# Kernel optimization log

Measured on AMD Instinct MI355X. Metric: run time of the kernel, lower is better.

The kernel has to match this reference:

```python
import jax, jax.numpy as jnp
import numpy as np

B, N, K, DIM = 2, 20000, 16, 256


def _mlp(x, W, b):
    # torch nn.Linear: x @ W.T + b, then LeakyReLU(0.1)
    return jax.nn.leaky_relu(x @ W.T + b, negative_slope=0.1)


def _lfa(features, geom, idx, W, b):
    # features: [B, N, C]; geom: [B, N, K, 4]; idx: [B, N, K]
    t = _mlp(geom, W, b)                                  # [B, N, K, d_lfa]
    fn = jax.vmap(lambda f, i: f[i])(features, idx)       # gather neighbors: [B, N, K, C]
    # mean over K of concat == concat of means (faithful, avoids big concat)
    return jnp.concatenate([t.mean(axis=2), fn.mean(axis=2)], axis=-1)


def _linear_init(key, out_f, in_f):
    k1, k2 = jax.random.split(key)
    bound = 1.0 / np.sqrt(in_f)
    W = jax.random.uniform(k1, (out_f, in_f), jnp.float32, -bound, bound)
    b = jax.random.uniform(k2, (out_f,), jnp.float32, -bound, bound)
    return W, b


def setup_inputs() -> dict:
    key = jax.random.key(0)
    ks = jax.random.split(key, 8)
    W_init, b_init = _linear_init(ks[0], DIM // 4, DIM)
    W_l1, b_l1 = _linear_init(ks[1], DIM // 4, 4)
    W_l2, b_l2 = _linear_init(ks[2], DIM // 2, 4)
    W_fin, b_fin = _linear_init(ks[3], DIM, DIM)
    W_id, b_id = _linear_init(ks[4], DIM, DIM)
    return {
        "input_tensor": jax.random.normal(ks[5], (B, N, DIM), jnp.float32),
        "geometric_features": jax.random.normal(ks[6], (B, N, K, 4), jnp.float32),
        "neighbor_indices": jax.random.randint(ks[7], (B, N, K), 0, N, jnp.int64 if jax.config.jax_enable_x64 else jnp.int32),
        "W_init": W_init, "b_init": b_init,
        "W_l1": W_l1, "b_l1": b_l1,
        "W_l2": W_l2, "b_l2": b_l2,
        "W_fin": W_fin, "b_fin": b_fin,
        "W_id": W_id, "b_id": b_id,
    }


def reference(input_tensor, geometric_features, neighbor_indices,
              W_init, b_init, W_l1, b_l1, W_l2, b_l2,
              W_fin, b_fin, W_id, b_id):
    residual = input_tensor
    x = _mlp(input_tensor, W_init, b_init)                       # [B, N, dim/4]
    x = _lfa(x, geometric_features, neighbor_indices, W_l1, b_l1)  # [B, N, dim/2]
    x = _lfa(x, geometric_features, neighbor_indices, W_l2, b_l2)  # [B, N, dim]
    x = _mlp(x, W_fin, b_fin)
    return x + _mlp(residual, W_id, b_id)
```

## Files before the change

### kernel.cpp

```cpp
#include <hip/hip_runtime.h>
#include <hip/hip_bf16.h>

#define BN   40000
#define NPTS 20000
#define KNN  16
#define DIM  256

typedef __attribute__((ext_vector_type(8))) short bf16x8;
typedef __attribute__((ext_vector_type(4))) float f32x4;
typedef __attribute__((ext_vector_type(16))) float f32x16;

__device__ __forceinline__ float lrelu(float v) { return fmaxf(v, 0.1f * v); }
__device__ __forceinline__ float bs2f(short s) {
    union { unsigned u; float f; } c; c.u = ((unsigned)(unsigned short)s) << 16;
    return c.f;
}
__device__ __forceinline__ short f2bs(float f) {
    __hip_bfloat16 h = __float2bfloat16(f);
    return *reinterpret_cast<short*>(&h);
}
__device__ __forceinline__ bf16x8 ldf32_bf16x8(const float* p) {
    const float4 a = ((const float4*)p)[0];
    const float4 b = ((const float4*)p)[1];
    bf16x8 r;
    r[0]=f2bs(a.x); r[1]=f2bs(a.y); r[2]=f2bs(a.z); r[3]=f2bs(a.w);
    r[4]=f2bs(b.x); r[5]=f2bs(b.y); r[6]=f2bs(b.z); r[7]=f2bs(b.w);
    return r;
}

__device__ __forceinline__ void dma16(const void* g, void* l) {
    __builtin_amdgcn_global_load_lds(
        (const __attribute__((address_space(1))) unsigned int*)g,
        (__attribute__((address_space(3))) unsigned int*)l, 16, 0, 0);
}

__global__ void __launch_bounds__(256) prep_kernel(
    const int* __restrict__ idxw, int* __restrict__ flag,
    const float* __restrict__ Wf, const float* __restrict__ Wi,
    const float* __restrict__ Wn,
    short* __restrict__ Wt, short* __restrict__ Wnt)
{
    if (blockIdx.x == 0) {
        __shared__ int red[256];
        int t = threadIdx.x;
        int v = 0;
#pragma unroll
        for (int it = 0; it < 64; ++it)
            v |= idxw[2 * (t + it * 256) + 1];
        red[t] = v;
        __syncthreads();
        for (int s = 128; s > 0; s >>= 1) {
            if (t < s) red[t] |= red[t + s];
            __syncthreads();
        }
        if (t == 0) *flag = (red[0] != 0) ? 1 : 0;
        return;
    }
    int t = (blockIdx.x - 1) * 256 + threadIdx.x;
    if (t < 32768) {
        int mat = (t >> 14) & 1;
        int tt  = t & 16383;
        float4 v = mat ? ((const float4*)Wi)[tt] : ((const float4*)Wf)[tt];
        int n  = tt >> 6;
        int k  = (tt & 63) * 4;
        int kk = k >> 5, q = (k >> 3) & 3, j = k & 7;
        short4 o; o.x=f2bs(v.x); o.y=f2bs(v.y); o.z=f2bs(v.z); o.w=f2bs(v.w);
        *(short4*)(Wt + ((size_t)((kk*2 + mat)*4 + q))*2048 + n*8 + j) = o;
    } else {
        int tt = t - 32768;
        float4 v = ((const float4*)Wn)[tt];
        int n  = tt >> 6;
        int k  = (tt & 63) * 4;
        int kk = k >> 5, q = (k >> 3) & 3, j = k & 7;
        short4 o; o.x=f2bs(v.x); o.y=f2bs(v.y); o.z=f2bs(v.z); o.w=f2bs(v.w);
        *(short4*)(Wnt + ((size_t)((kk*4 + q)*64 + n))*8 + j) = o;
    }
}

__global__ void __launch_bounds__(256) stage2_kernel(
    const float* __restrict__ geom,
    const float* __restrict__ W1, const float* __restrict__ B1,
    const float* __restrict__ W2, const float* __restrict__ B2,
    const float* __restrict__ X,
    const short* __restrict__ Wnt,
    const float* __restrict__ b_init,
    __hip_bfloat16* __restrict__ x2,
    __hip_bfloat16* __restrict__ x3,
    __hip_bfloat16* __restrict__ x1)
{
    __shared__ short wbuf[16384];

    if (blockIdx.x >= 625) {
        int bid = blockIdx.x - 625;
        int t = threadIdx.x;
        int wave = t >> 6, lane = t & 63;
        int r = lane & 15, q = lane >> 4;
        {
            const char* W8 = (const char*)Wnt;
            char* L8 = (char*)wbuf;
#pragma unroll
            for (int rd = 0; rd < 8; ++rd) {
                int off = (wave * 8 + rd) * 1024 + lane * 16;
                dma16(W8 + off, L8 + off);
            }
        }
        int m0 = bid * 64 + wave * 16;
        const float* Xs = X + (size_t)(m0 + r) * DIM + q * 8;
        bf16x8 a[8];
#pragma unroll
        for (int kk = 0; kk < 8; ++kk) a[kk] = ldf32_bf16x8(Xs + kk * 32);
        __syncthreads();

        f32x4 acc[4];
#pragma unroll
        for (int nt = 0; nt < 4; ++nt) acc[nt] = (f32x4){0.f,0.f,0.f,0.f};
#pragma unroll
        for (int kk = 0; kk < 8; ++kk) {
#pragma unroll
            for (int nt = 0; nt < 4; ++nt) {
                bf16x8 b = *(const bf16x8*)&wbuf[((kk*4 + q)*64 + nt*16 + r) * 8];
                acc[nt] = __builtin_amdgcn_mfma_f32_16x16x32_bf16(a[kk], b, acc[nt], 0, 0, 0);
            }
        }
#pragma unroll
        for (int nt = 0; nt < 4; ++nt) {
            int col = nt * 16 + r;
            float bvx = b_init[col];
#pragma unroll
            for (int i = 0; i < 4; ++i) {
                float v = lrelu(acc[nt][i] + bvx);
                x1[(size_t)(m0 + q*4 + i) * 64 + col] = __float2bfloat16(v);
            }
        }
        return;
    }

    const int lane = threadIdx.x & 63;
    const int wv   = threadIdx.x >> 6;
    const int c31  = lane & 31;
    const int hi   = lane >> 5;
    const int wglob = blockIdx.x * 4 + wv;

    bf16x8 bfr[6]; float bv[6];
#pragma unroll
    for (int tt = 0; tt < 6; ++tt) {
        bfr[tt] = (bf16x8){0,0,0,0,0,0,0,0};
        const float* Wrow;
        if (tt < 2) { Wrow = W1 + (size_t)(tt*32 + c31) * 4;     bv[tt] = B1[tt*32 + c31]; }
        else        { Wrow = W2 + (size_t)((tt-2)*32 + c31) * 4; bv[tt] = B2[(tt-2)*32 + c31]; }
        if (hi == 0) {
            const float4 w4 = *(const float4*)Wrow;
            bfr[tt][0]=f2bs(w4.x); bfr[tt][1]=f2bs(w4.y);
            bfr[tt][2]=f2bs(w4.z); bfr[tt][3]=f2bs(w4.w);
        }
    }
    f32x16 ZR;
#pragma unroll
    for (int i = 0; i < 16; ++i) ZR[i] = 0.f;

    float4 g = (float4){0.f,0.f,0.f,0.f};
    if (hi == 0)
        g = *(const float4*)(geom +
            ((size_t)((wglob * 8) * 2 + (c31 >> 4)) * KNN + (c31 & 15)) * 4);

#pragma unroll
    for (int it = 0; it < 8; ++it) {
        const int p0 = (wglob * 8 + it) * 2;
        const float4 gc = g;
        if (it < 7 && hi == 0)
            g = *(const float4*)(geom +
                ((size_t)(p0 + 2 + (c31 >> 4)) * KNN + (c31 & 15)) * 4);

        bf16x8 a = (bf16x8){0,0,0,0,0,0,0,0};
        if (hi == 0) { a[0]=f2bs(gc.x); a[1]=f2bs(gc.y); a[2]=f2bs(gc.z); a[3]=f2bs(gc.w); }

        f32x16 acc[6];
#pragma unroll
        for (int tt = 0; tt < 6; ++tt)
            acc[tt] = __builtin_amdgcn_mfma_f32_32x32x16_bf16(a, bfr[tt], ZR, 0, 0, 0);

#pragma unroll
        for (int tt = 0; tt < 6; ++tt) {
            float sA = 0.f, sB = 0.f;
#pragma unroll
            for (int i = 0; i < 8; ++i)  sA += lrelu(acc[tt][i]     + bv[tt]);
#pragma unroll
            for (int i = 0; i < 8; ++i)  sB += lrelu(acc[tt][i + 8] + bv[tt]);
            sA += __shfl_xor(sA, 32, 64);
            sB += __shfl_xor(sB, 32, 64);
            const float s = (hi ? sB : sA) * (1.f / 16.f);
            const short v = f2bs(s);
            if (tt < 2) ((short*)x2)[(size_t)(p0 + hi) * 128 + tt*32 + c31] = v;
            else        ((short*)x3)[(size_t)(p0 + hi) * 256 + (tt-2)*32 + c31] = v;
        }
    }
}

__global__ void __launch_bounds__(256) gather1_kernel(
    const int* __restrict__ idxw, const int* __restrict__ flag,
    const __hip_bfloat16* __restrict__ x1,
    __hip_bfloat16* __restrict__ x2)
{
    int t = blockIdx.x * 256 + threadIdx.x;
    int p = t >> 3, j = t & 7;
    int lane = threadIdx.x & 63;
    int dual = (*flag == 0) ? 2 : 1;
    int base = (p >= NPTS) ? NPTS : 0;
    int i0 = idxw[((size_t)p * 16 + 2*j)     * dual];
    int i1 = idxw[((size_t)p * 16 + 2*j + 1) * dual];
    int g8 = lane & 56;
    float acc[8];
#pragma unroll
    for (int i = 0; i < 8; ++i) acc[i] = 0.f;
#pragma unroll
    for (int k = 0; k < 8; ++k) {
        int rA = base + __shfl(i0, g8 + k, 64);
        int rB = base + __shfl(i1, g8 + k, 64);
        bf16x8 vA = *(const bf16x8*)((const short*)x1 + (size_t)rA * 64 + j * 8);
        bf16x8 vB = *(const bf16x8*)((const short*)x1 + (size_t)rB * 64 + j * 8);
#pragma unroll
        for (int i = 0; i < 8; ++i) acc[i] += bs2f(vA[i]) + bs2f(vB[i]);
    }
    bf16x8 o;
#pragma unroll
    for (int i = 0; i < 8; ++i) o[i] = f2bs(acc[i] * (1.f/16.f));
    *(bf16x8*)((short*)x2 + (size_t)p * 128 + 64 + j * 8) = o;
}

__global__ void __launch_bounds__(256) gather2_kernel(
    const int* __restrict__ idxw, const int* __restrict__ flag,
    const __hip_bfloat16* __restrict__ x2,
    __hip_bfloat16* __restrict__ x3)
{
    int t = blockIdx.x * 256 + threadIdx.x;
    int p = t >> 4, j = t & 15;
    int lane = threadIdx.x & 63;
    int dual = (*flag == 0) ? 2 : 1;
    int base = (p >= NPTS) ? NPTS : 0;
    int myi = idxw[((size_t)p * 16 + j) * dual];
    int g16 = lane & 48;
    float acc[8];
#pragma unroll
    for (int i = 0; i < 8; ++i) acc[i] = 0.f;
#pragma unroll
    for (int k = 0; k < KNN; ++k) {
        int row = base + __shfl(myi, g16 + k, 64);
        bf16x8 v = *(const bf16x8*)((const short*)x2 + (size_t)row * 128 + j * 8);
#pragma unroll
        for (int i = 0; i < 8; ++i) acc[i] += bs2f(v[i]);
    }
    bf16x8 o;
#pragma unroll
    for (int i = 0; i < 8; ++i) o[i] = f2bs(acc[i] * (1.f/16.f));
    *(bf16x8*)((short*)x3 + (size_t)p * 256 + 128 + j * 8) = o;
}

__global__ void __launch_bounds__(512, 2) final_mfma(
    const __hip_bfloat16* __restrict__ X3,
    const float* __restrict__ RES,
    const short* __restrict__ Wt,
    const float* __restrict__ Bf,
    const float* __restrict__ Bi,
    float* __restrict__ OUT)
{
    __shared__ short lw[65536];
    const int t    = threadIdx.x;
    const int wave = t >> 6, lane = t & 63;
    const int r = lane & 15, q = lane >> 4;
    const int rg = wave >> 1, cg = wave & 1;
    const int ch = blockIdx.x & 1;
    const int p0 = (blockIdx.x >> 1) * 320;

    {
        const char* WtB = (const char*)Wt;
        char* L = (char*)lw;
#pragma unroll
        for (int i = 0; i < 16; ++i) {
            int c = wave * 8 + (i >> 1);
            int d = i & 1;
            int mat = c >> 5, kk = (c >> 2) & 7, qq = c & 3;
            int src_sh = ((kk * 2 + mat) * 4 + qq) * 2048 + ch * 1024;
            dma16(WtB + (size_t)src_sh * 2 + d * 1024 + lane * 16,
                  L + (c * 2 + d) * 1024 + lane * 16);
        }
    }
    const int cb = ch * 128 + cg * 64;
    float bfv[4], biv[4];
#pragma unroll
    for (int nt = 0; nt < 4; ++nt) {
        bfv[nt] = Bf[cb + nt * 16 + r];
        biv[nt] = Bi[cb + nt * 16 + r];
    }
    __syncthreads();

    const short* bpf = lw + q * 1024 + (cg * 64 + r) * 8;
    const short* bpi = bpf + 32768;

#pragma unroll
    for (int tt = 0; tt < 5; ++tt) {
        const int row = p0 + tt * 64 + rg * 16 + r;
        const short* x3r = (const short*)X3 + (size_t)row * DIM + q * 8;
        const float* rsr = RES + (size_t)row * DIM + q * 8;

        bf16x8 a1[8];
        float4 rw[16];
#pragma unroll
        for (int kk = 0; kk < 8; ++kk) {
            rw[2*kk]   = ((const float4*)rsr)[kk * 8];
            rw[2*kk+1] = ((const float4*)rsr)[kk * 8 + 1];
            a1[kk] = *(const bf16x8*)(x3r + kk * 32);
        }

        f32x4 acc1[4], acc2[4];
#pragma unroll
        for (int nt = 0; nt < 4; ++nt) {
            acc1[nt] = (f32x4){0.f,0.f,0.f,0.f};
            acc2[nt] = (f32x4){0.f,0.f,0.f,0.f};
        }
#pragma unroll
        for (int kk = 0; kk < 8; ++kk) {
            bf16x8 a2;
            {
                const float4 lo = rw[2*kk], hi = rw[2*kk+1];
                a2[0]=f2bs(lo.x); a2[1]=f2bs(lo.y); a2[2]=f2bs(lo.z); a2[3]=f2bs(lo.w);
                a2[4]=f2bs(hi.x); a2[5]=f2bs(hi.y); a2[6]=f2bs(hi.z); a2[7]=f2bs(hi.w);
            }
#pragma unroll
            for (int nt = 0; nt < 4; ++nt) {
                bf16x8 b1 = *(const bf16x8*)(bpf + kk * 4096 + nt * 128);
                bf16x8 b2 = *(const bf16x8*)(bpi + kk * 4096 + nt * 128);
                acc1[nt] = __builtin_amdgcn_mfma_f32_16x16x32_bf16(a1[kk], b1, acc1[nt], 0, 0, 0);
                acc2[nt] = __builtin_amdgcn_mfma_f32_16x16x32_bf16(a2,    b2, acc2[nt], 0, 0, 0);
            }
        }
#pragma unroll
        for (int nt = 0; nt < 4; ++nt) {
            const int col = cb + nt * 16 + r;
#pragma unroll
            for (int i = 0; i < 4; ++i) {
                float v = lrelu(acc1[nt][i] + bfv[nt]) + lrelu(acc2[nt][i] + biv[nt]);
                OUT[(size_t)(p0 + tt * 64 + rg * 16 + q * 4 + i) * DIM + col] = v;
            }
        }
    }
}

extern "C" void kernel_launch(void* const* d_in, const int* in_sizes, int n_in,
                              void* d_out, int out_size, void* d_ws, size_t ws_size,
                              hipStream_t stream)
{
    const float* input  = (const float*)d_in[0];
    const float* geom   = (const float*)d_in[1];
    const int*   idxw   = (const int*)d_in[2];
    const float* W_init = (const float*)d_in[3];
    const float* b_init = (const float*)d_in[4];
    const float* W_l1   = (const float*)d_in[5];
    const float* b_l1   = (const float*)d_in[6];
    const float* W_l2   = (const float*)d_in[7];
    const float* b_l2   = (const float*)d_in[8];
    const float* W_fin  = (const float*)d_in[9];
    const float* b_fin  = (const float*)d_in[10];
    const float* W_id   = (const float*)d_in[11];
    const float* b_id   = (const float*)d_in[12];
    float* out = (float*)d_out;

    char* ws = (char*)d_ws;
    int* flag = (int*)ws;
    short* Wt  = (short*)(ws + 16);
    short* Wnt = (short*)(ws + 16 + 262144);
    __hip_bfloat16* x2 = (__hip_bfloat16*)(ws + 16 + 5120000);
    __hip_bfloat16* x3 = (__hip_bfloat16*)(ws + 16 + 15360000);
    __hip_bfloat16* x1 = (__hip_bfloat16*)d_out;

    prep_kernel<<<145, 256, 0, stream>>>(idxw, flag, W_fin, W_id, W_init,
                                         Wt, Wnt);
    stage2_kernel<<<1250, 256, 0, stream>>>(geom, W_l1, b_l1, W_l2, b_l2,
                                            input, Wnt, b_init, x2, x3, x1);
    gather1_kernel<<<1250, 256, 0, stream>>>(idxw, flag, x1, x2);
    gather2_kernel<<<2500, 256, 0, stream>>>(idxw, flag, x2, x3);
    final_mfma<<<250, 512, 0, stream>>>(x3, input, Wt, b_fin, b_id, out);
}
```

Measured before the change: 195.8 us.

## Fuse second neighbor gather into final MFMA kernel via shared-memory staging

Removes the separate gather2 kernel and computes the second-LFA neighbor mean inside the final GEMM kernel. Each 64-row tile is staged in LDS, and x3 now stores only its 128 MLP columns, so the round trip of the gathered half through global memory goes away. Each block of 250 redundantly gathers its tile for both column halves, since ch splits output columns. Occupancy is lowered to 1 block per CU by extra LDS and launch bounds, and the tile loop is no longer unrolled, with two syncs per iteration.

```diff
diff --git a/kernel.cpp b/kernel.cpp
--- a/kernel.cpp
+++ b/kernel.cpp
@@ -191,7 +191,7 @@
             const float s = (hi ? sB : sA) * (1.f / 16.f);
             const short v = f2bs(s);
             if (tt < 2) ((short*)x2)[(size_t)(p0 + hi) * 128 + tt*32 + c31] = v;
-            else        ((short*)x3)[(size_t)(p0 + hi) * 256 + (tt-2)*32 + c31] = v;
+            else        ((short*)x3)[(size_t)(p0 + hi) * 128 + (tt-2)*32 + c31] = v;
         }
     }
 }
@@ -227,36 +227,10 @@
     *(bf16x8*)((short*)x2 + (size_t)p * 128 + 64 + j * 8) = o;
 }
 
-__global__ void __launch_bounds__(256) gather2_kernel(
+__global__ void __launch_bounds__(512, 1) final_mfma(
+    const __hip_bfloat16* __restrict__ X3g,
+    const __hip_bfloat16* __restrict__ X2,
     const int* __restrict__ idxw, const int* __restrict__ flag,
-    const __hip_bfloat16* __restrict__ x2,
-    __hip_bfloat16* __restrict__ x3)
-{
-    int t = blockIdx.x * 256 + threadIdx.x;
-    int p = t >> 4, j = t & 15;
-    int lane = threadIdx.x & 63;
-    int dual = (*flag == 0) ? 2 : 1;
-    int base = (p >= NPTS) ? NPTS : 0;
-    int myi = idxw[((size_t)p * 16 + j) * dual];
-    int g16 = lane & 48;
-    float acc[8];
-#pragma unroll
-    for (int i = 0; i < 8; ++i) acc[i] = 0.f;
-#pragma unroll
-    for (int k = 0; k < KNN; ++k) {
-        int row = base + __shfl(myi, g16 + k, 64);
-        bf16x8 v = *(const bf16x8*)((const short*)x2 + (size_t)row * 128 + j * 8);
-#pragma unroll
-        for (int i = 0; i < 8; ++i) acc[i] += bs2f(v[i]);
-    }
-    bf16x8 o;
-#pragma unroll
-    for (int i = 0; i < 8; ++i) o[i] = f2bs(acc[i] * (1.f/16.f));
-    *(bf16x8*)((short*)x3 + (size_t)p * 256 + 128 + j * 8) = o;
-}
-
-__global__ void __launch_bounds__(512, 2) final_mfma(
-    const __hip_bfloat16* __restrict__ X3,
     const float* __restrict__ RES,
     const short* __restrict__ Wt,
     const float* __restrict__ Bf,
@@ -264,12 +238,14 @@
     float* __restrict__ OUT)
 {
     __shared__ short lw[65536];
+    __shared__ short x3h[64 * 136];
     const int t    = threadIdx.x;
     const int wave = t >> 6, lane = t & 63;
     const int r = lane & 15, q = lane >> 4;
     const int rg = wave >> 1, cg = wave & 1;
     const int ch = blockIdx.x & 1;
     const int p0 = (blockIdx.x >> 1) * 320;
+    const int dual = (*flag == 0) ? 2 : 1;
 
     {
         const char* WtB = (const char*)Wt;
@@ -291,15 +267,15 @@
         bfv[nt] = Bf[cb + nt * 16 + r];
         biv[nt] = Bi[cb + nt * 16 + r];
     }
-    __syncthreads();
 
     const short* bpf = lw + q * 1024 + (cg * 64 + r) * 8;
     const short* bpi = bpf + 32768;
-
-#pragma unroll
+    const int jg  = t & 15;
+    const int g16 = lane & 48;
+
+#pragma unroll 1
     for (int tt = 0; tt < 5; ++tt) {
         const int row = p0 + tt * 64 + rg * 16 + r;
-        const short* x3r = (const short*)X3 + (size_t)row * DIM + q * 8;
         const float* rsr = RES + (size_t)row * DIM + q * 8;
 
         bf16x8 a1[8];
@@ -308,8 +284,44 @@
         for (int kk = 0; kk < 8; ++kk) {
             rw[2*kk]   = ((const float4*)rsr)[kk * 8];
             rw[2*kk+1] = ((const float4*)rsr)[kk * 8 + 1];
-            a1[kk] = *(const bf16x8*)(x3r + kk * 32);
-        }
+        }
+        {
+            const short* x3r = (const short*)X3g + (size_t)row * 128 + q * 8;
+#pragma unroll
+            for (int kk = 0; kk < 4; ++kk)
+                a1[kk] = *(const bf16x8*)(x3r + kk * 32);
+        }
+
+#pragma unroll
+        for (int pass = 0; pass < 2; ++pass) {
+            const int rl = (t >> 4) + pass * 32;
+            const int p  = p0 + tt * 64 + rl;
+            const int base = (p >= NPTS) ? NPTS : 0;
+            const int myi = idxw[((size_t)p * 16 + jg) * dual];
+            float ac[8];
+#pragma unroll
+            for (int i = 0; i < 8; ++i) ac[i] = 0.f;
+#pragma unroll
+            for (int k = 0; k < KNN; ++k) {
+                int nbr = base + __shfl(myi, g16 + k, 64);
+                bf16x8 v = *(const bf16x8*)((const short*)X2 + (size_t)nbr * 128 + jg * 8);
+#pragma unroll
+                for (int i = 0; i < 8; ++i) ac[i] += bs2f(v[i]);
+            }
+            bf16x8 o;
+#pragma unroll
+            for (int i = 0; i < 8; ++i) o[i] = f2bs(ac[i] * (1.f/16.f));
+            *(bf16x8*)&x3h[rl * 136 + jg * 8] = o;
+        }
+        __syncthreads();
+
+        {
+            const short* xh = x3h + (rg * 16 + r) * 136 + q * 8;
+#pragma unroll
+            for (int kk = 4; kk < 8; ++kk)
+                a1[kk] = *(const bf16x8*)(xh + (kk - 4) * 32);
+        }
+        __syncthreads();
 
         f32x4 acc1[4], acc2[4];
 #pragma unroll
@@ -321,9 +333,9 @@
         for (int kk = 0; kk < 8; ++kk) {
             bf16x8 a2;
             {
-                const float4 lo = rw[2*kk], hi = rw[2*kk+1];
-                a2[0]=f2bs(lo.x); a2[1]=f2bs(lo.y); a2[2]=f2bs(lo.z); a2[3]=f2bs(lo.w);
-                a2[4]=f2bs(hi.x); a2[5]=f2bs(hi.y); a2[6]=f2bs(hi.z); a2[7]=f2bs(hi.w);
+                const float4 lo = rw[2*kk], hi2 = rw[2*kk+1];
+                a2[0]=f2bs(lo.x);  a2[1]=f2bs(lo.y);  a2[2]=f2bs(lo.z);  a2[3]=f2bs(lo.w);
+                a2[4]=f2bs(hi2.x); a2[5]=f2bs(hi2.y); a2[6]=f2bs(hi2.z); a2[7]=f2bs(hi2.w);
             }
 #pragma unroll
             for (int nt = 0; nt < 4; ++nt) {
@@ -377,6 +389,6 @@
     stage2_kernel<<<1250, 256, 0, stream>>>(geom, W_l1, b_l1, W_l2, b_l2,
                                             input, Wnt, b_init, x2, x3, x1);
     gather1_kernel<<<1250, 256, 0, stream>>>(idxw, flag, x1, x2);
-    gather2_kernel<<<2500, 256, 0, stream>>>(idxw, flag, x2, x3);
-    final_mfma<<<250, 512, 0, stream>>>(x3, input, Wt, b_fin, b_id, out);
-}
+    final_mfma<<<250, 512, 0, stream>>>(x3, x2, idxw, flag, input,
+                                        Wt, b_fin, b_id, out);
+}
```

New measurement: 224.7 us. +14.8%, slower.

## Fuse all five stages into one cooperative persistent kernel with grid syncs

Applied to the files above, without the earlier changes.

Replaces the five separate kernel launches (weight prep, geometry MLP plus init GEMM, two gathers, final GEMM) with a single cooperative kernel of 250 blocks of 512 threads. Stages are separated by grid.sync. The aim is to remove launch gaps and tail effects between kernels. In exchange, occupancy drops to one large block per CU with 128KB of LDS, the loops are less unrolled, and each stage uses a fixed work split that may balance worse than the old per-kernel grids. The x1 buffer still aliases the output, which is only safe because the final stage writes OUT after the gathers.

```diff
diff --git a/kernel.cpp b/kernel.cpp
--- a/kernel.cpp
+++ b/kernel.cpp
@@ -1,5 +1,8 @@
 #include <hip/hip_runtime.h>
 #include <hip/hip_bf16.h>
+#include <hip/hip_cooperative_groups.h>
+
+namespace cg = cooperative_groups;
 
 #define BN   40000
 #define NPTS 20000
@@ -34,246 +37,199 @@
         (__attribute__((address_space(3))) unsigned int*)l, 16, 0, 0);
 }
 
-__global__ void __launch_bounds__(256) prep_kernel(
-    const int* __restrict__ idxw, int* __restrict__ flag,
-    const float* __restrict__ Wf, const float* __restrict__ Wi,
-    const float* __restrict__ Wn,
-    short* __restrict__ Wt, short* __restrict__ Wnt)
-{
-    if (blockIdx.x == 0) {
-        __shared__ int red[256];
-        int t = threadIdx.x;
-        int v = 0;
-#pragma unroll
-        for (int it = 0; it < 64; ++it)
-            v |= idxw[2 * (t + it * 256) + 1];
-        red[t] = v;
-        __syncthreads();
-        for (int s = 128; s > 0; s >>= 1) {
-            if (t < s) red[t] |= red[t + s];
-            __syncthreads();
-        }
-        if (t == 0) *flag = (red[0] != 0) ? 1 : 0;
-        return;
-    }
-    int t = (blockIdx.x - 1) * 256 + threadIdx.x;
-    if (t < 32768) {
-        int mat = (t >> 14) & 1;
-        int tt  = t & 16383;
-        float4 v = mat ? ((const float4*)Wi)[tt] : ((const float4*)Wf)[tt];
-        int n  = tt >> 6;
-        int k  = (tt & 63) * 4;
-        int kk = k >> 5, q = (k >> 3) & 3, j = k & 7;
-        short4 o; o.x=f2bs(v.x); o.y=f2bs(v.y); o.z=f2bs(v.z); o.w=f2bs(v.w);
-        *(short4*)(Wt + ((size_t)((kk*2 + mat)*4 + q))*2048 + n*8 + j) = o;
-    } else {
-        int tt = t - 32768;
-        float4 v = ((const float4*)Wn)[tt];
-        int n  = tt >> 6;
-        int k  = (tt & 63) * 4;
-        int kk = k >> 5, q = (k >> 3) & 3, j = k & 7;
-        short4 o; o.x=f2bs(v.x); o.y=f2bs(v.y); o.z=f2bs(v.z); o.w=f2bs(v.w);
-        *(short4*)(Wnt + ((size_t)((kk*4 + q)*64 + n))*8 + j) = o;
-    }
-}
-
-__global__ void __launch_bounds__(256) stage2_kernel(
+__global__ void __launch_bounds__(512, 1) mega_kernel(
     const float* __restrict__ geom,
     const float* __restrict__ W1, const float* __restrict__ B1,
     const float* __restrict__ W2, const float* __restrict__ B2,
     const float* __restrict__ X,
-    const short* __restrict__ Wnt,
+    const int* __restrict__ idxw,
+    const float* __restrict__ Wf, const float* __restrict__ Wi,
+    const float* __restrict__ Wn,
     const float* __restrict__ b_init,
+    const float* __restrict__ Bf, const float* __restrict__ Bi,
+    short* __restrict__ Wt, short* __restrict__ Wnt,
+    int* __restrict__ flagp,
+    __hip_bfloat16* __restrict__ x1,
     __hip_bfloat16* __restrict__ x2,
     __hip_bfloat16* __restrict__ x3,
-    __hip_bfloat16* __restrict__ x1)
-{
-    __shared__ short wbuf[16384];
-
-    if (blockIdx.x >= 625) {
-        int bid = blockIdx.x - 625;
-        int t = threadIdx.x;
-        int wave = t >> 6, lane = t & 63;
-        int r = lane & 15, q = lane >> 4;
-        {
-            const char* W8 = (const char*)Wnt;
-            char* L8 = (char*)wbuf;
-#pragma unroll
-            for (int rd = 0; rd < 8; ++rd) {
-                int off = (wave * 8 + rd) * 1024 + lane * 16;
-                dma16(W8 + off, L8 + off);
-            }
-        }
-        int m0 = bid * 64 + wave * 16;
-        const float* Xs = X + (size_t)(m0 + r) * DIM + q * 8;
-        bf16x8 a[8];
-#pragma unroll
-        for (int kk = 0; kk < 8; ++kk) a[kk] = ldf32_bf16x8(Xs + kk * 32);
-        __syncthreads();
-
-        f32x4 acc[4];
-#pragma unroll
-        for (int nt = 0; nt < 4; ++nt) acc[nt] = (f32x4){0.f,0.f,0.f,0.f};
-#pragma unroll
-        for (int kk = 0; kk < 8; ++kk) {
-#pragma unroll
-            for (int nt = 0; nt < 4; ++nt) {
-                bf16x8 b = *(const bf16x8*)&wbuf[((kk*4 + q)*64 + nt*16 + r) * 8];
-                acc[nt] = __builtin_amdgcn_mfma_f32_16x16x32_bf16(a[kk], b, acc[nt], 0, 0, 0);
-            }
-        }
-#pragma unroll
-        for (int nt = 0; nt < 4; ++nt) {
-            int col = nt * 16 + r;
-            float bvx = b_init[col];
-#pragma unroll
-            for (int i = 0; i < 4; ++i) {
-                float v = lrelu(acc[nt][i] + bvx);
-                x1[(size_t)(m0 + q*4 + i) * 64 + col] = __float2bfloat16(v);
-            }
-        }
-        return;
-    }
-
-    const int lane = threadIdx.x & 63;
-    const int wv   = threadIdx.x >> 6;
-    const int c31  = lane & 31;
-    const int hi   = lane >> 5;
-    const int wglob = blockIdx.x * 4 + wv;
-
-    bf16x8 bfr[6]; float bv[6];
-#pragma unroll
-    for (int tt = 0; tt < 6; ++tt) {
-        bfr[tt] = (bf16x8){0,0,0,0,0,0,0,0};
-        const float* Wrow;
-        if (tt < 2) { Wrow = W1 + (size_t)(tt*32 + c31) * 4;     bv[tt] = B1[tt*32 + c31]; }
-        else        { Wrow = W2 + (size_t)((tt-2)*32 + c31) * 4; bv[tt] = B2[(tt-2)*32 + c31]; }
-        if (hi == 0) {
-            const float4 w4 = *(const float4*)Wrow;
-            bfr[tt][0]=f2bs(w4.x); bfr[tt][1]=f2bs(w4.y);
-            bfr[tt][2]=f2bs(w4.z); bfr[tt][3]=f2bs(w4.w);
-        }
-    }
-    f32x16 ZR;
-#pragma unroll
-    for (int i = 0; i < 16; ++i) ZR[i] = 0.f;
-
-    float4 g = (float4){0.f,0.f,0.f,0.f};
-    if (hi == 0)
-        g = *(const float4*)(geom +
-            ((size_t)((wglob * 8) * 2 + (c31 >> 4)) * KNN + (c31 & 15)) * 4);
-
-#pragma unroll
-    for (int it = 0; it < 8; ++it) {
-        const int p0 = (wglob * 8 + it) * 2;
-        const float4 gc = g;
-        if (it < 7 && hi == 0)
-            g = *(const float4*)(geom +
-                ((size_t)(p0 + 2 + (c31 >> 4)) * KNN + (c31 & 15)) * 4);
-
-        bf16x8 a = (bf16x8){0,0,0,0,0,0,0,0};
-        if (hi == 0) { a[0]=f2bs(gc.x); a[1]=f2bs(gc.y); a[2]=f2bs(gc.z); a[3]=f2bs(gc.w); }
-
-        f32x16 acc[6];
-#pragma unroll
-        for (int tt = 0; tt < 6; ++tt)
-            acc[tt] = __builtin_amdgcn_mfma_f32_32x32x16_bf16(a, bfr[tt], ZR, 0, 0, 0);
-
-#pragma unroll
-        for (int tt = 0; tt < 6; ++tt) {
-            float sA = 0.f, sB = 0.f;
-#pragma unroll
-            for (int i = 0; i < 8; ++i)  sA += lrelu(acc[tt][i]     + bv[tt]);
-#pragma unroll
-            for (int i = 0; i < 8; ++i)  sB += lrelu(acc[tt][i + 8] + bv[tt]);
-            sA += __shfl_xor(sA, 32, 64);
-            sB += __shfl_xor(sB, 32, 64);
-            const float s = (hi ? sB : sA) * (1.f / 16.f);
-            const short v = f2bs(s);
-            if (tt < 2) ((short*)x2)[(size_t)(p0 + hi) * 128 + tt*32 + c31] = v;
-            else        ((short*)x3)[(size_t)(p0 + hi) * 256 + (tt-2)*32 + c31] = v;
-        }
-    }
-}
-
-__global__ void __launch_bounds__(256) gather1_kernel(
-    const int* __restrict__ idxw, const int* __restrict__ flag,
-    const __hip_bfloat16* __restrict__ x1,
-    __hip_bfloat16* __restrict__ x2)
-{
-    int t = blockIdx.x * 256 + threadIdx.x;
-    int p = t >> 3, j = t & 7;
-    int lane = threadIdx.x & 63;
-    int dual = (*flag == 0) ? 2 : 1;
-    int base = (p >= NPTS) ? NPTS : 0;
-    int i0 = idxw[((size_t)p * 16 + 2*j)     * dual];
-    int i1 = idxw[((size_t)p * 16 + 2*j + 1) * dual];
-    int g8 = lane & 56;
-    float acc[8];
-#pragma unroll
-    for (int i = 0; i < 8; ++i) acc[i] = 0.f;
-#pragma unroll
-    for (int k = 0; k < 8; ++k) {
-        int rA = base + __shfl(i0, g8 + k, 64);
-        int rB = base + __shfl(i1, g8 + k, 64);
-        bf16x8 vA = *(const bf16x8*)((const short*)x1 + (size_t)rA * 64 + j * 8);
-        bf16x8 vB = *(const bf16x8*)((const short*)x1 + (size_t)rB * 64 + j * 8);
-#pragma unroll
-        for (int i = 0; i < 8; ++i) acc[i] += bs2f(vA[i]) + bs2f(vB[i]);
-    }
-    bf16x8 o;
-#pragma unroll
-    for (int i = 0; i < 8; ++i) o[i] = f2bs(acc[i] * (1.f/16.f));
-    *(bf16x8*)((short*)x2 + (size_t)p * 128 + 64 + j * 8) = o;
-}
-
-__global__ void __launch_bounds__(256) gather2_kernel(
-    const int* __restrict__ idxw, const int* __restrict__ flag,
-    const __hip_bfloat16* __restrict__ x2,
-    __hip_bfloat16* __restrict__ x3)
-{
-    int t = blockIdx.x * 256 + threadIdx.x;
-    int p = t >> 4, j = t & 15;
-    int lane = threadIdx.x & 63;
-    int dual = (*flag == 0) ? 2 : 1;
-    int base = (p >= NPTS) ? NPTS : 0;
-    int myi = idxw[((size_t)p * 16 + j) * dual];
-    int g16 = lane & 48;
-    float acc[8];
-#pragma unroll
-    for (int i = 0; i < 8; ++i) acc[i] = 0.f;
-#pragma unroll
-    for (int k = 0; k < KNN; ++k) {
-        int row = base + __shfl(myi, g16 + k, 64);
-        bf16x8 v = *(const bf16x8*)((const short*)x2 + (size_t)row * 128 + j * 8);
-#pragma unroll
-        for (int i = 0; i < 8; ++i) acc[i] += bs2f(v[i]);
-    }
-    bf16x8 o;
-#pragma unroll
-    for (int i = 0; i < 8; ++i) o[i] = f2bs(acc[i] * (1.f/16.f));
-    *(bf16x8*)((short*)x3 + (size_t)p * 256 + 128 + j * 8) = o;
-}
-
-__global__ void __launch_bounds__(512, 2) final_mfma(
-    const __hip_bfloat16* __restrict__ X3,
-    const float* __restrict__ RES,
-    const short* __restrict__ Wt,
-    const float* __restrict__ Bf,
-    const float* __restrict__ Bi,
     float* __restrict__ OUT)
 {
     __shared__ short lw[65536];
-    const int t    = threadIdx.x;
-    const int wave = t >> 6, lane = t & 63;
-    const int r = lane & 15, q = lane >> 4;
-    const int rg = wave >> 1, cg = wave & 1;
-    const int ch = blockIdx.x & 1;
-    const int p0 = (blockIdx.x >> 1) * 320;
+    __shared__ int dred[8];
+    cg::grid_group grid = cg::this_grid();
+    const int tid  = threadIdx.x;
+    const int wave = tid >> 6, lane = tid & 63;
+    const int bid  = blockIdx.x;
+
+    if (bid < 72) {
+        int t = bid * 512 + tid;
+        if (t < 32768) {
+            int mat = (t >> 14) & 1;
+            int tt  = t & 16383;
+            float4 v = mat ? ((const float4*)Wi)[tt] : ((const float4*)Wf)[tt];
+            int n  = tt >> 6;
+            int k  = (tt & 63) * 4;
+            int kk = k >> 5, q = (k >> 3) & 3, j = k & 7;
+            short4 o; o.x=f2bs(v.x); o.y=f2bs(v.y); o.z=f2bs(v.z); o.w=f2bs(v.w);
+            *(short4*)(Wt + ((size_t)((kk*2 + mat)*4 + q))*2048 + n*8 + j) = o;
+        } else {
+            int tt = t - 32768;
+            float4 v = ((const float4*)Wn)[tt];
+            int n  = tt >> 6;
+            int k  = (tt & 63) * 4;
+            int kk = k >> 5, q = (k >> 3) & 3, j = k & 7;
+            short4 o; o.x=f2bs(v.x); o.y=f2bs(v.y); o.z=f2bs(v.z); o.w=f2bs(v.w);
+            *(short4*)(Wnt + ((size_t)((kk*4 + q)*64 + n))*8 + j) = o;
+        }
+    } else if (bid == 72) {
+        int v = 0;
+#pragma unroll
+        for (int it = 0; it < 32; ++it)
+            v |= idxw[2 * (tid + it * 512) + 1];
+#pragma unroll
+        for (int s = 1; s < 64; s <<= 1) v |= __shfl_xor(v, s, 64);
+        if (lane == 0) dred[wave] = v;
+        __syncthreads();
+        if (tid == 0) {
+            int r0 = 0;
+#pragma unroll
+            for (int i = 0; i < 8; ++i) r0 |= dred[i];
+            *flagp = (r0 != 0) ? 1 : 0;
+        }
+    }
+    grid.sync();
+    const int dual = (*(volatile const int*)flagp == 0) ? 2 : 1;
+
+    {
+        {
+            const char* W8 = (const char*)Wnt;
+            char* L8 = (char*)lw;
+#pragma unroll
+            for (int rd = 0; rd < 4; ++rd) {
+                int off = (wave * 4 + rd) * 1024 + lane * 16;
+                dma16(W8 + off, L8 + off);
+            }
+        }
+        const int c31 = lane & 31;
+        const int hi  = lane >> 5;
+        const int wglob = bid * 8 + wave;
+        bf16x8 bfr[6]; float bv[6];
+#pragma unroll
+        for (int tt = 0; tt < 6; ++tt) {
+            bfr[tt] = (bf16x8){0,0,0,0,0,0,0,0};
+            const float* Wrow;
+            if (tt < 2) { Wrow = W1 + (size_t)(tt*32 + c31) * 4;     bv[tt] = B1[tt*32 + c31]; }
+            else        { Wrow = W2 + (size_t)((tt-2)*32 + c31) * 4; bv[tt] = B2[(tt-2)*32 + c31]; }
+            if (hi == 0) {
+                const float4 w4 = *(const float4*)Wrow;
+                bfr[tt][0]=f2bs(w4.x); bfr[tt][1]=f2bs(w4.y);
+                bfr[tt][2]=f2bs(w4.z); bfr[tt][3]=f2bs(w4.w);
+            }
+        }
+        f32x16 ZR;
+#pragma unroll
+        for (int i = 0; i < 16; ++i) ZR[i] = 0.f;
+
+        float4 g = (float4){0.f,0.f,0.f,0.f};
+        if (hi == 0)
+            g = *(const float4*)(geom +
+                ((size_t)((wglob * 10) * 2 + (c31 >> 4)) * KNN + (c31 & 15)) * 4);
+#pragma unroll 1
+        for (int it = 0; it < 10; ++it) {
+            const int pg = (wglob * 10 + it) * 2;
+            const float4 gc = g;
+            if (it < 9 && hi == 0)
+                g = *(const float4*)(geom +
+                    ((size_t)(pg + 2 + (c31 >> 4)) * KNN + (c31 & 15)) * 4);
+            bf16x8 a = (bf16x8){0,0,0,0,0,0,0,0};
+            if (hi == 0) { a[0]=f2bs(gc.x); a[1]=f2bs(gc.y); a[2]=f2bs(gc.z); a[3]=f2bs(gc.w); }
+            f32x16 acc[6];
+#pragma unroll
+            for (int tt = 0; tt < 6; ++tt)
+                acc[tt] = __builtin_amdgcn_mfma_f32_32x32x16_bf16(a, bfr[tt], ZR, 0, 0, 0);
+#pragma unroll
+            for (int tt = 0; tt < 6; ++tt) {
+                float sA = 0.f, sB = 0.f;
+#pragma unroll
+                for (int i = 0; i < 8; ++i)  sA += lrelu(acc[tt][i]     + bv[tt]);
+#pragma unroll
+                for (int i = 0; i < 8; ++i)  sB += lrelu(acc[tt][i + 8] + bv[tt]);
+                sA += __shfl_xor(sA, 32, 64);
+                sB += __shfl_xor(sB, 32, 64);
+                const float s = (hi ? sB : sA) * (1.f / 16.f);
+                const short v = f2bs(s);
+                if (tt < 2) ((short*)x2)[(size_t)(pg + hi) * 128 + tt*32 + c31] = v;
+                else        ((short*)x3)[(size_t)(pg + hi) * 256 + (tt-2)*32 + c31] = v;
+            }
+        }
+        __syncthreads();
+
+        const int r = lane & 15, q = lane >> 4;
+#pragma unroll 1
+        for (int ti = wave; ti < 10; ti += 8) {
+            const int m0 = bid * 160 + ti * 16;
+            const float* Xs = X + (size_t)(m0 + r) * DIM + q * 8;
+            bf16x8 a[8];
+#pragma unroll
+            for (int kk = 0; kk < 8; ++kk) a[kk] = ldf32_bf16x8(Xs + kk * 32);
+            f32x4 acc[4];
+#pragma unroll
+            for (int nt = 0; nt < 4; ++nt) acc[nt] = (f32x4){0.f,0.f,0.f,0.f};
+#pragma unroll
+            for (int kk = 0; kk < 8; ++kk) {
+#pragma unroll
+                for (int nt = 0; nt < 4; ++nt) {
+                    bf16x8 b = *(const bf16x8*)&lw[((kk*4 + q)*64 + nt*16 + r) * 8];
+                    acc[nt] = __builtin_amdgcn_mfma_f32_16x16x32_bf16(a[kk], b, acc[nt], 0, 0, 0);
+                }
+            }
+#pragma unroll
+            for (int nt = 0; nt < 4; ++nt) {
+                int col = nt * 16 + r;
+                float bvx = b_init[col];
+#pragma unroll
+                for (int i = 0; i < 4; ++i) {
+                    float v = lrelu(acc[nt][i] + bvx);
+                    x1[(size_t)(m0 + q*4 + i) * 64 + col] = __float2bfloat16(v);
+                }
+            }
+        }
+    }
+    grid.sync();
+
+#pragma unroll 1
+    for (int it = 0; it < 3; ++it) {
+        int t = bid * 512 + tid + it * 128000;
+        if (t < 320000) {
+            int p = t >> 3, j = t & 7;
+            int base = (p >= NPTS) ? NPTS : 0;
+            int i0 = idxw[((size_t)p * 16 + 2*j)     * dual];
+            int i1 = idxw[((size_t)p * 16 + 2*j + 1) * dual];
+            int g8 = lane & 56;
+            float acc[8];
+#pragma unroll
+            for (int i = 0; i < 8; ++i) acc[i] = 0.f;
+#pragma unroll
+            for (int k = 0; k < 8; ++k) {
+                int rA = base + __shfl(i0, g8 + k, 64);
+                int rB = base + __shfl(i1, g8 + k, 64);
+                bf16x8 vA = *(const bf16x8*)((const short*)x1 + (size_t)rA * 64 + j * 8);
+                bf16x8 vB = *(const bf16x8*)((const short*)x1 + (size_t)rB * 64 + j * 8);
+#pragma unroll
+                for (int i = 0; i < 8; ++i) acc[i] += bs2f(vA[i]) + bs2f(vB[i]);
+            }
+            bf16x8 o;
+#pragma unroll
+            for (int i = 0; i < 8; ++i) o[i] = f2bs(acc[i] * (1.f/16.f));
+            *(bf16x8*)((short*)x2 + (size_t)p * 128 + 64 + j * 8) = o;
+        }
+    }
+    grid.sync();
 
     {
         const char* WtB = (const char*)Wt;
         char* L = (char*)lw;
+        const int ch = bid & 1;
 #pragma unroll
         for (int i = 0; i < 16; ++i) {
             int c = wave * 8 + (i >> 1);
@@ -284,62 +240,90 @@
                   L + (c * 2 + d) * 1024 + lane * 16);
         }
     }
-    const int cb = ch * 128 + cg * 64;
-    float bfv[4], biv[4];
-#pragma unroll
-    for (int nt = 0; nt < 4; ++nt) {
-        bfv[nt] = Bf[cb + nt * 16 + r];
-        biv[nt] = Bi[cb + nt * 16 + r];
+#pragma unroll 1
+    for (int it = 0; it < 5; ++it) {
+        int t = bid * 512 + tid + it * 128000;
+        int p = t >> 4, j = t & 15;
+        int base = (p >= NPTS) ? NPTS : 0;
+        int myi = idxw[((size_t)p * 16 + j) * dual];
+        int g16 = lane & 48;
+        float acc[8];
+#pragma unroll
+        for (int i = 0; i < 8; ++i) acc[i] = 0.f;
+#pragma unroll
+        for (int k = 0; k < KNN; ++k) {
+            int row = base + __shfl(myi, g16 + k, 64);
+            bf16x8 v = *(const bf16x8*)((const short*)x2 + (size_t)row * 128 + j * 8);
+#pragma unroll
+            for (int i = 0; i < 8; ++i) acc[i] += bs2f(v[i]);
+        }
+        bf16x8 o;
+#pragma unroll
+        for (int i = 0; i < 8; ++i) o[i] = f2bs(acc[i] * (1.f/16.f));
+        *(bf16x8*)((short*)x3 + (size_t)p * 256 + 128 + j * 8) = o;
     }
     __syncthreads();
-
-    const short* bpf = lw + q * 1024 + (cg * 64 + r) * 8;
-    const short* bpi = bpf + 32768;
-
-#pragma unroll
-    for (int tt = 0; tt < 5; ++tt) {
-        const int row = p0 + tt * 64 + rg * 16 + r;
-        const short* x3r = (const short*)X3 + (size_t)row * DIM + q * 8;
-        const float* rsr = RES + (size_t)row * DIM + q * 8;
-
-        bf16x8 a1[8];
-        float4 rw[16];
-#pragma unroll
-        for (int kk = 0; kk < 8; ++kk) {
-            rw[2*kk]   = ((const float4*)rsr)[kk * 8];
-            rw[2*kk+1] = ((const float4*)rsr)[kk * 8 + 1];
-            a1[kk] = *(const bf16x8*)(x3r + kk * 32);
-        }
-
-        f32x4 acc1[4], acc2[4];
+    grid.sync();
+
+    {
+        const int r = lane & 15, q = lane >> 4;
+        const int rg = wave >> 1, cgp = wave & 1;
+        const int ch = bid & 1;
+        const int p0 = (bid >> 1) * 320;
+        const int cb = ch * 128 + cgp * 64;
+        float bfv[4], biv[4];
 #pragma unroll
         for (int nt = 0; nt < 4; ++nt) {
-            acc1[nt] = (f32x4){0.f,0.f,0.f,0.f};
-            acc2[nt] = (f32x4){0.f,0.f,0.f,0.f};
-        }
-#pragma unroll
-        for (int kk = 0; kk < 8; ++kk) {
-            bf16x8 a2;
-            {
-                const float4 lo = rw[2*kk], hi = rw[2*kk+1];
-                a2[0]=f2bs(lo.x); a2[1]=f2bs(lo.y); a2[2]=f2bs(lo.z); a2[3]=f2bs(lo.w);
-                a2[4]=f2bs(hi.x); a2[5]=f2bs(hi.y); a2[6]=f2bs(hi.z); a2[7]=f2bs(hi.w);
-            }
+            bfv[nt] = Bf[cb + nt * 16 + r];
+            biv[nt] = Bi[cb + nt * 16 + r];
+        }
+        const short* bpf = lw + q * 1024 + (cgp * 64 + r) * 8;
+        const short* bpi = bpf + 32768;
+
+#pragma unroll 1
+        for (int tt = 0; tt < 5; ++tt) {
+            const int row = p0 + tt * 64 + rg * 16 + r;
+            const short* x3r = (const short*)x3 + (size_t)row * DIM + q * 8;
+            const float* rsr = X + (size_t)row * DIM + q * 8;
+
+            bf16x8 a1[8];
+            float4 rw[16];
+#pragma unroll
+            for (int kk = 0; kk < 8; ++kk) {
+                rw[2*kk]   = ((const float4*)rsr)[kk * 8];
+                rw[2*kk+1] = ((const float4*)rsr)[kk * 8 + 1];
+                a1[kk] = *(const bf16x8*)(x3r + kk * 32);
+            }
+            f32x4 acc1[4], acc2[4];
 #pragma unroll
             for (int nt = 0; nt < 4; ++nt) {
-                bf16x8 b1 = *(const bf16x8*)(bpf + kk * 4096 + nt * 128);
-                bf16x8 b2 = *(const bf16x8*)(bpi + kk * 4096 + nt * 128);
-                acc1[nt] = __builtin_amdgcn_mfma_f32_16x16x32_bf16(a1[kk], b1, acc1[nt], 0, 0, 0);
-                acc2[nt] = __builtin_amdgcn_mfma_f32_16x16x32_bf16(a2,    b2, acc2[nt], 0, 0, 0);
-            }
-        }
-#pragma unroll
-        for (int nt = 0; nt < 4; ++nt) {
-            const int col = cb + nt * 16 + r;
-#pragma unroll
-            for (int i = 0; i < 4; ++i) {
-                float v = lrelu(acc1[nt][i] + bfv[nt]) + lrelu(acc2[nt][i] + biv[nt]);
-                OUT[(size_t)(p0 + tt * 64 + rg * 16 + q * 4 + i) * DIM + col] = v;
+                acc1[nt] = (f32x4){0.f,0.f,0.f,0.f};
+                acc2[nt] = (f32x4){0.f,0.f,0.f,0.f};
+            }
+#pragma unroll
+            for (int kk = 0; kk < 8; ++kk) {
+                bf16x8 a2;
+                {
+                    const float4 lo = rw[2*kk], hi2 = rw[2*kk+1];
+                    a2[0]=f2bs(lo.x);  a2[1]=f2bs(lo.y);  a2[2]=f2bs(lo.z);  a2[3]=f2bs(lo.w);
+                    a2[4]=f2bs(hi2.x); a2[5]=f2bs(hi2.y); a2[6]=f2bs(hi2.z); a2[7]=f2bs(hi2.w);
+                }
+#pragma unroll
+                for (int nt = 0; nt < 4; ++nt) {
+                    bf16x8 b1 = *(const bf16x8*)(bpf + kk * 4096 + nt * 128);
+                    bf16x8 b2 = *(const bf16x8*)(bpi + kk * 4096 + nt * 128);
+                    acc1[nt] = __builtin_amdgcn_mfma_f32_16x16x32_bf16(a1[kk], b1, acc1[nt], 0, 0, 0);
+                    acc2[nt] = __builtin_amdgcn_mfma_f32_16x16x32_bf16(a2,    b2, acc2[nt], 0, 0, 0);
+                }
+            }
+#pragma unroll
+            for (int nt = 0; nt < 4; ++nt) {
+                const int col = cb + nt * 16 + r;
+#pragma unroll
+                for (int i = 0; i < 4; ++i) {
+                    float v = lrelu(acc1[nt][i] + bfv[nt]) + lrelu(acc2[nt][i] + biv[nt]);
+                    OUT[(size_t)(p0 + tt * 64 + rg * 16 + q * 4 + i) * DIM + col] = v;
+                }
             }
         }
     }
@@ -372,11 +356,14 @@
     __hip_bfloat16* x3 = (__hip_bfloat16*)(ws + 16 + 15360000);
     __hip_bfloat16* x1 = (__hip_bfloat16*)d_out;
 
-    prep_kernel<<<145, 256, 0, stream>>>(idxw, flag, W_fin, W_id, W_init,
-                                         Wt, Wnt);
-    stage2_kernel<<<1250, 256, 0, stream>>>(geom, W_l1, b_l1, W_l2, b_l2,
-                                            input, Wnt, b_init, x2, x3, x1);
-    gather1_kernel<<<1250, 256, 0, stream>>>(idxw, flag, x1, x2);
-    gather2_kernel<<<2500, 256, 0, stream>>>(idxw, flag, x2, x3);
-    final_mfma<<<250, 512, 0, stream>>>(x3, input, Wt, b_fin, b_id, out);
-}
+    void* args[] = {
+        (void*)&geom, (void*)&W_l1, (void*)&b_l1, (void*)&W_l2, (void*)&b_l2,
+        (void*)&input, (void*)&idxw,
+        (void*)&W_fin, (void*)&W_id, (void*)&W_init,
+        (void*)&b_init, (void*)&b_fin, (void*)&b_id,
+        (void*)&Wt, (void*)&Wnt, (void*)&flag,
+        (void*)&x1, (void*)&x2, (void*)&x3, (void*)&out
+    };
+    hipLaunchCooperativeKernel((void*)mega_kernel, dim3(250), dim3(512),
+                               args, 0, stream);
+}
```

Result: slower. 379.8 us (+94.0%).

## Split final GEMM into four column quarters per block and batch init-MLP loads

Applied to the files above, without the earlier changes.

The final fused dual-GEMM kernel now launches 500 blocks of 256 threads, each handling a 64-column quarter of the output with 64 KB of LDS weights instead of 128 KB. This raises block count and occupancy, at the cost of every input row being read by four blocks instead of two. The init MLP path in stage2 also issues all fp32 loads for a half of the row before converting them to bf16, which should expose more memory-level parallelism.

```diff
diff --git a/kernel.cpp b/kernel.cpp
--- a/kernel.cpp
+++ b/kernel.cpp
@@ -105,10 +105,25 @@
             }
         }
         int m0 = bid * 64 + wave * 16;
-        const float* Xs = X + (size_t)(m0 + r) * DIM + q * 8;
+        const float4* X4 = (const float4*)(X + (size_t)(m0 + r) * DIM + q * 8);
         bf16x8 a[8];
 #pragma unroll
-        for (int kk = 0; kk < 8; ++kk) a[kk] = ldf32_bf16x8(Xs + kk * 32);
+        for (int g = 0; g < 2; ++g) {
+            float4 rwm[8];
+#pragma unroll
+            for (int kk = 0; kk < 4; ++kk) {
+                rwm[2*kk]   = X4[(g*4 + kk) * 8];
+                rwm[2*kk+1] = X4[(g*4 + kk) * 8 + 1];
+            }
+#pragma unroll
+            for (int kk = 0; kk < 4; ++kk) {
+                const float4 lo = rwm[2*kk], hi2 = rwm[2*kk+1];
+                bf16x8 av;
+                av[0]=f2bs(lo.x);  av[1]=f2bs(lo.y);  av[2]=f2bs(lo.z);  av[3]=f2bs(lo.w);
+                av[4]=f2bs(hi2.x); av[5]=f2bs(hi2.y); av[6]=f2bs(hi2.z); av[7]=f2bs(hi2.w);
+                a[g*4 + kk] = av;
+            }
+        }
         __syncthreads();
 
         f32x4 acc[4];
@@ -255,7 +270,7 @@
     *(bf16x8*)((short*)x3 + (size_t)p * 256 + 128 + j * 8) = o;
 }
 
-__global__ void __launch_bounds__(512, 2) final_mfma(
+__global__ void __launch_bounds__(256, 2) final_mfma(
     const __hip_bfloat16* __restrict__ X3,
     const float* __restrict__ RES,
     const short* __restrict__ Wt,
@@ -263,28 +278,26 @@
     const float* __restrict__ Bi,
     float* __restrict__ OUT)
 {
-    __shared__ short lw[65536];
+    __shared__ short lw[32768];
     const int t    = threadIdx.x;
     const int wave = t >> 6, lane = t & 63;
     const int r = lane & 15, q = lane >> 4;
-    const int rg = wave >> 1, cg = wave & 1;
-    const int ch = blockIdx.x & 1;
-    const int p0 = (blockIdx.x >> 1) * 320;
+    const int cq = blockIdx.x & 3;
+    const int p0 = (blockIdx.x >> 2) * 320;
 
     {
         const char* WtB = (const char*)Wt;
         char* L = (char*)lw;
 #pragma unroll
         for (int i = 0; i < 16; ++i) {
-            int c = wave * 8 + (i >> 1);
-            int d = i & 1;
+            int c = wave * 16 + i;
             int mat = c >> 5, kk = (c >> 2) & 7, qq = c & 3;
-            int src_sh = ((kk * 2 + mat) * 4 + qq) * 2048 + ch * 1024;
-            dma16(WtB + (size_t)src_sh * 2 + d * 1024 + lane * 16,
-                  L + (c * 2 + d) * 1024 + lane * 16);
-        }
-    }
-    const int cb = ch * 128 + cg * 64;
+            int s = ((kk * 2 + mat) * 4 + qq);
+            dma16(WtB + (size_t)s * 4096 + cq * 1024 + lane * 16,
+                  L + c * 1024 + lane * 16);
+        }
+    }
+    const int cb = cq * 64;
     float bfv[4], biv[4];
 #pragma unroll
     for (int nt = 0; nt < 4; ++nt) {
@@ -293,12 +306,12 @@
     }
     __syncthreads();
 
-    const short* bpf = lw + q * 1024 + (cg * 64 + r) * 8;
-    const short* bpi = bpf + 32768;
+    const short* bpf = lw + q * 512 + r * 8;
+    const short* bpi = bpf + 16384;
 
 #pragma unroll
     for (int tt = 0; tt < 5; ++tt) {
-        const int row = p0 + tt * 64 + rg * 16 + r;
+        const int row = p0 + tt * 64 + wave * 16 + r;
         const short* x3r = (const short*)X3 + (size_t)row * DIM + q * 8;
         const float* rsr = RES + (size_t)row * DIM + q * 8;
 
@@ -321,14 +334,14 @@
         for (int kk = 0; kk < 8; ++kk) {
             bf16x8 a2;
             {
-                const float4 lo = rw[2*kk], hi = rw[2*kk+1];
-                a2[0]=f2bs(lo.x); a2[1]=f2bs(lo.y); a2[2]=f2bs(lo.z); a2[3]=f2bs(lo.w);
-                a2[4]=f2bs(hi.x); a2[5]=f2bs(hi.y); a2[6]=f2bs(hi.z); a2[7]=f2bs(hi.w);
+                const float4 lo = rw[2*kk], hi2 = rw[2*kk+1];
+                a2[0]=f2bs(lo.x);  a2[1]=f2bs(lo.y);  a2[2]=f2bs(lo.z);  a2[3]=f2bs(lo.w);
+                a2[4]=f2bs(hi2.x); a2[5]=f2bs(hi2.y); a2[6]=f2bs(hi2.z); a2[7]=f2bs(hi2.w);
             }
 #pragma unroll
             for (int nt = 0; nt < 4; ++nt) {
-                bf16x8 b1 = *(const bf16x8*)(bpf + kk * 4096 + nt * 128);
-                bf16x8 b2 = *(const bf16x8*)(bpi + kk * 4096 + nt * 128);
+                bf16x8 b1 = *(const bf16x8*)(bpf + kk * 2048 + nt * 128);
+                bf16x8 b2 = *(const bf16x8*)(bpi + kk * 2048 + nt * 128);
                 acc1[nt] = __builtin_amdgcn_mfma_f32_16x16x32_bf16(a1[kk], b1, acc1[nt], 0, 0, 0);
                 acc2[nt] = __builtin_amdgcn_mfma_f32_16x16x32_bf16(a2,    b2, acc2[nt], 0, 0, 0);
             }
@@ -339,7 +352,7 @@
 #pragma unroll
             for (int i = 0; i < 4; ++i) {
                 float v = lrelu(acc1[nt][i] + bfv[nt]) + lrelu(acc2[nt][i] + biv[nt]);
-                OUT[(size_t)(p0 + tt * 64 + rg * 16 + q * 4 + i) * DIM + col] = v;
+                OUT[(size_t)(p0 + tt * 64 + wave * 16 + q * 4 + i) * DIM + col] = v;
             }
         }
     }
@@ -378,5 +391,5 @@
                                             input, Wnt, b_init, x2, x3, x1);
     gather1_kernel<<<1250, 256, 0, stream>>>(idxw, flag, x1, x2);
     gather2_kernel<<<2500, 256, 0, stream>>>(idxw, flag, x2, x3);
-    final_mfma<<<250, 512, 0, stream>>>(x3, input, Wt, b_fin, b_id, out);
-}
+    final_mfma<<<500, 256, 0, stream>>>(x3, input, Wt, b_fin, b_id, out);
+}
```

Measured after the change: 210.4 us. 7.4% more time.
